# Kernel tuning notes

Hardware: AMD Instinct MI355X
Metric: run time of the kernel (lower is better)

Reference implementation:

```python
import jax, jax.numpy as jnp
import numpy as np

N = 20000   # nodes
E = 320000  # edges (before self-loops)
D = 256     # feature width (inChl = hdChl = outChl)
H = 4       # heads
C = D // H  # per-head channels = 64
NEG_SLOPE = 0.2
LN_EPS = 1e-5


def setup_inputs() -> dict:
    key = jax.random.key(0)
    ks = jax.random.split(key, 2 + 4 * 4)
    inp = {}
    inp["x"] = jax.random.normal(ks[0], (1, N, D), dtype=jnp.float32)
    inp["edge_index"] = jax.random.randint(ks[1], (2, E), 0, N, dtype=jnp.int32)
    s = 1.0 / np.sqrt(D)
    for i in range(4):
        k = 2 + 4 * i
        inp[f"Wl{i+1}"] = (jax.random.normal(ks[k], (D, H * C), dtype=jnp.float32) * s)
        inp[f"Wr{i+1}"] = (jax.random.normal(ks[k + 1], (D, H * C), dtype=jnp.float32) * s)
        inp[f"att{i+1}"] = (jax.random.normal(ks[k + 2], (H, C), dtype=jnp.float32) * s)
        inp[f"b{i+1}"] = jnp.zeros((H * C,), dtype=jnp.float32)
        inp[f"g{i+1}"] = jnp.ones((D,), dtype=jnp.float32)
        inp[f"be{i+1}"] = jnp.zeros((D,), dtype=jnp.float32)
    return inp


def _segment_softmax(scores, seg, num_segments):
    # scores: [E, H], per-destination softmax over incoming edges
    m = jax.ops.segment_max(scores, seg, num_segments=num_segments)
    e = jnp.exp(scores - m[seg])
    d = jax.ops.segment_sum(e, seg, num_segments=num_segments)
    return e / d[seg]


def _gatv2(x, src, dst, Wl, Wr, att, b):
    # GATv2Conv defaults: share_weights=False, concat=True, negative_slope=0.2
    n = x.shape[0]
    xl = (x @ Wl).reshape(n, H, C)  # source transform
    xr = (x @ Wr).reshape(n, H, C)  # target transform
    m = xl[src] + xr[dst]                                  # [E', H, C]
    e = jnp.sum(jax.nn.leaky_relu(m, NEG_SLOPE) * att, -1) # [E', H]
    alpha = _segment_softmax(e, dst, n)                    # [E', H]
    out = jax.ops.segment_sum(xl[src] * alpha[:, :, None], dst, num_segments=n)
    return out.reshape(n, H * C) + b


def _layernorm(x, g, b):
    mu = jnp.mean(x, -1, keepdims=True)
    var = jnp.mean(jnp.square(x - mu), -1, keepdims=True)
    return (x - mu) * jax.lax.rsqrt(var + LN_EPS) * g + b


def _forward(x, edge_index, layers):
    h = x[0]  # squeeze batch dim -> [N, D]
    n = h.shape[0]
    loop = jnp.arange(n, dtype=edge_index.dtype)
    src = jnp.concatenate([edge_index[0], loop])  # add_self_loops=True
    dst = jnp.concatenate([edge_index[1], loop])
    for (Wl, Wr, att, b, g, be) in layers:
        h = _gatv2(h, src, dst, Wl, Wr, att, b)
        h = jax.nn.relu(_layernorm(h, g, be))
    return h[None]  # unsqueeze -> [1, N, D]


def reference(x, edge_index,
              Wl1, Wr1, att1, b1, g1, be1,
              Wl2, Wr2, att2, b2, g2, be2,
              Wl3, Wr3, att3, b3, g3, be3,
              Wl4, Wr4, att4, b4, g4, be4):
    layers = [(Wl1, Wr1, att1, b1, g1, be1),
              (Wl2, Wr2, att2, b2, g2, be2),
              (Wl3, Wr3, att3, b3, g3, be3),
              (Wl4, Wr4, att4, b4, g4, be4)]
    return _forward(x, edge_index, layers)
```

## Files before the change

kernel.cpp:

```cpp
#include <hip/hip_runtime.h>
#include <math.h>

#define N_NODES 20000
#define E_EDGES 320000
#define EP (E_EDGES + N_NODES)
#define D 256
#define NHEAD 4
#define CH 64
#define NEG_SLOPE 0.2f
#define LN_EPS 1e-5f

typedef _Float16 half8_t __attribute__((ext_vector_type(8)));
typedef _Float16 half4_t __attribute__((ext_vector_type(4)));
typedef _Float16 half2_t __attribute__((ext_vector_type(2)));
typedef float   float4_t __attribute__((ext_vector_type(4)));

#define SCATTER_BLOCKS ((EP + 255) / 256)

__device__ __forceinline__ void async_cp16(const void* g, void* l)
{
    __builtin_amdgcn_global_load_lds(
        (const __attribute__((address_space(1))) void*)g,
        (__attribute__((address_space(3))) void*)l, 16, 0, 0);
}

template<int CTRL>
__device__ __forceinline__ float dpp_add(float v) {
    int t = __builtin_amdgcn_update_dpp(0, __float_as_int(v), CTRL, 0xF, 0xF, true);
    return v + __int_as_float(t);
}
__device__ __forceinline__ float row_sum16(float v) {
    v = dpp_add<0x121>(v);
    v = dpp_add<0x122>(v);
    v = dpp_add<0x124>(v);
    v = dpp_add<0x128>(v);
    return v;
}

__global__ __launch_bounds__(256)
void convert_hist_kernel(const float* __restrict__ x, _Float16* __restrict__ h16,
                         const int* __restrict__ ei, int* __restrict__ deg)
{
    int i = blockIdx.x * 256 + threadIdx.x;
    if (i < EP) {
        int dst = (i < E_EDGES) ? ei[E_EDGES + i] : (i - E_EDGES);
        atomicAdd(&deg[dst], 1);
    }
    if (i >= N_NODES * D / 4) return;
    float4 v = reinterpret_cast<const float4*>(x)[i];
    half4_t o;
    o.x = (_Float16)v.x; o.y = (_Float16)v.y; o.z = (_Float16)v.z; o.w = (_Float16)v.w;
    reinterpret_cast<half4_t*>(h16)[i] = o;
}

__global__ __launch_bounds__(1024)
void csr_scan_kernel(const int* __restrict__ deg, int* __restrict__ rowptr,
                     int* __restrict__ cursor, int* __restrict__ csr_src)
{
    __shared__ int wsum[16];
    int t = threadIdx.x, lane = t & 63, w = t >> 6;
    if (t < 8) csr_src[EP + t] = 0;
    int base = t * 20;
    int loc[20];
    int s = 0;
    #pragma unroll
    for (int k = 0; k < 20; ++k) {
        int idx = base + k;
        loc[k] = (idx < N_NODES) ? deg[idx] : 0;
        s += loc[k];
    }
    int x = s;
    #pragma unroll
    for (int o = 1; o < 64; o <<= 1) {
        int y = __shfl_up(x, o, 64);
        if (lane >= o) x += y;
    }
    if (lane == 63) wsum[w] = x;
    __syncthreads();
    if (t == 0) {
        int sacc = 0;
        #pragma unroll
        for (int k = 0; k < 16; ++k) { int tmp = wsum[k]; wsum[k] = sacc; sacc += tmp; }
        rowptr[N_NODES] = sacc;
    }
    __syncthreads();
    int excl = wsum[w] + x - s;
    #pragma unroll
    for (int k = 0; k < 20; ++k) {
        int idx = base + k;
        if (idx < N_NODES) { rowptr[idx] = excl; cursor[idx] = excl; }
        excl += loc[k];
    }
}

struct WPtrs { const float* p[8]; };
__global__ __launch_bounds__(256)
void scatter_convw_kernel(const int* __restrict__ ei, int* __restrict__ cursor,
                          int* __restrict__ csr_src, WPtrs wp,
                          _Float16* __restrict__ Wt_all)
{
    if (blockIdx.x < SCATTER_BLOCKS) {
        int e = blockIdx.x * 256 + threadIdx.x;
        if (e >= EP) return;
        int src, dst;
        if (e < E_EDGES) { src = ei[e]; dst = ei[E_EDGES + e]; }
        else             { src = dst = e - E_EDGES; }
        int pos = atomicAdd(&cursor[dst], 1);
        csr_src[pos] = src;
        return;
    }
    __shared__ float tile[64][65];
    int bz = blockIdx.x - SCATTER_BLOCKS;
    int bxi = bz & 3, byi = (bz >> 2) & 3, z = bz >> 4;
    const float* W = wp.p[z];
    _Float16* out = Wt_all + (size_t)z * 65536;
    int bx = bxi * 64, by = byi * 64;
    int t = threadIdx.x;
    #pragma unroll
    for (int i = 0; i < 16; ++i) {
        int idx = t + i * 256;
        int kk = idx >> 6, nn = idx & 63;
        tile[kk][nn] = W[(by + kk) * 256 + bx + nn];
    }
    __syncthreads();
    #pragma unroll
    for (int i = 0; i < 16; ++i) {
        int idx = t + i * 256;
        int nn = idx >> 6, kk = idx & 63;
        out[(bx + nn) * 256 + by + kk] = (_Float16)tile[kk][nn];
    }
}

#define BM 128
#define BN 128
#define BK 64
#define EPAD2 72
__global__ __launch_bounds__(256)
void gemm_f16_kernel(const _Float16* __restrict__ A16, const _Float16* __restrict__ Wt,
                     _Float16* __restrict__ X0, _Float16* __restrict__ X1, int nrows)
{
    const _Float16* W = Wt + blockIdx.z * 65536 + blockIdx.y * (BN * 256);
    _Float16* X = blockIdx.z ? X1 : X0;
    const int row0 = blockIdx.x * BM;
    const int col0 = blockIdx.y * BN;

    __shared__ __align__(1024) char smem[BM * BK * 2 + BN * BK * 2];
    _Float16 (*As)[BK] = reinterpret_cast<_Float16 (*)[BK]>(smem);
    _Float16 (*Bs)[BK] = reinterpret_cast<_Float16 (*)[BK]>(smem + BM * BK * 2);
    _Float16* As_flat = reinterpret_cast<_Float16*>(smem);
    _Float16* Bs_flat = reinterpret_cast<_Float16*>(smem + BM * BK * 2);
    _Float16* ep = reinterpret_cast<_Float16*>(smem);

    const int tid  = threadIdx.x;
    const int wave = tid >> 6, lane = tid & 63;
    const int wy = wave >> 1, wx = wave & 1;
    const int quad = lane >> 4, l16 = lane & 15;

    float4_t acc[4][4];
    #pragma unroll
    for (int i = 0; i < 4; ++i)
        #pragma unroll
        for (int j = 0; j < 4; ++j) acc[i][j] = (float4_t)0.0f;

    const int r_in  = lane >> 3;
    const int c_in  = (lane & 7) * 8;

    #pragma unroll
    for (int k0 = 0; k0 < 256; k0 += BK) {
        #pragma unroll
        for (int j = 0; j < 4; ++j) {
            int ia  = wave * 4 + j;
            int row = ia * 8 + r_in;
            int gra = row0 + row;
            gra = (gra < nrows) ? gra : (nrows - 1);
            async_cp16(A16 + (size_t)gra * 256 + k0 + c_in, As_flat + ia * 512);
            async_cp16(W   + (size_t)row * 256 + k0 + c_in, Bs_flat + ia * 512);
        }
        __syncthreads();

        #pragma unroll
        for (int s = 0; s < 2; ++s) {
            half8_t af[4], bf[4];
            #pragma unroll
            for (int i = 0; i < 4; ++i)
                af[i] = *reinterpret_cast<const half8_t*>(&As[wy * 64 + i * 16 + l16][s * 32 + quad * 8]);
            #pragma unroll
            for (int j = 0; j < 4; ++j)
                bf[j] = *reinterpret_cast<const half8_t*>(&Bs[wx * 64 + j * 16 + l16][s * 32 + quad * 8]);
            #pragma unroll
            for (int i = 0; i < 4; ++i)
                #pragma unroll
                for (int j = 0; j < 4; ++j)
                    acc[i][j] = __builtin_amdgcn_mfma_f32_16x16x32_f16(af[i], bf[j], acc[i][j], 0, 0, 0);
        }
        __syncthreads();
    }

    _Float16* epw = ep + wave * 16 * EPAD2;
    #pragma unroll
    for (int it = 0; it < 4; ++it) {
        #pragma unroll
        for (int j = 0; j < 4; ++j)
            #pragma unroll
            for (int r = 0; r < 4; ++r)
                epw[(quad * 4 + r) * EPAD2 + j * 16 + l16] = (_Float16)acc[it][j][r];
        #pragma unroll
        for (int p = 0; p < 2; ++p) {
            int row = p * 8 + (lane >> 3);
            int col = (lane & 7) * 8;
            int gr = row0 + wy * 64 + it * 16 + row;
            half8_t v = *reinterpret_cast<const half8_t*>(&epw[row * EPAD2 + col]);
            if (gr < nrows)
                *reinterpret_cast<half8_t*>(X + gr * 256 + col0 + wx * 64 + col) = v;
        }
    }
}

__global__ __launch_bounds__(256)
void gat_fused_kernel(const _Float16* __restrict__ xl, const _Float16* __restrict__ xr,
                      const int* __restrict__ rowptr, const int* __restrict__ csr_src,
                      const float* __restrict__ att,
                      const float* __restrict__ bias, const float* __restrict__ g,
                      const float* __restrict__ be,
                      float* __restrict__ out32, _Float16* __restrict__ out16,
                      int write32)
{
    const int tid = threadIdx.x;
    const int w = tid >> 6, lane = tid & 63;
    const int n = blockIdx.x * 4 + w;
    const int start = rowptr[n], end = rowptr[n + 1];
    const int c0 = lane * 4;

    half2_t xr01, xr23, att01, att23;
    {
        half4_t xh = *reinterpret_cast<const half4_t*>(xr + n * D + c0);
        xr01.x = xh.x; xr01.y = xh.y; xr23.x = xh.z; xr23.y = xh.w;
        float4 av = *reinterpret_cast<const float4*>(att + c0);
        att01.x = (_Float16)av.x; att01.y = (_Float16)av.y;
        att23.x = (_Float16)av.z; att23.y = (_Float16)av.w;
    }
    const half2_t k02 = {(_Float16)NEG_SLOPE, (_Float16)NEG_SLOPE};

    float den = 0.0f;
    float4 num = make_float4(0.0f, 0.0f, 0.0f, 0.0f);

    int i = start;
    for (; i + 8 <= end; i += 8) {
        int sidx[8];
        #pragma unroll
        for (int j = 0; j < 8; ++j) sidx[j] = csr_src[i + j];
        half4_t h[8];
        #pragma unroll
        for (int j = 0; j < 8; ++j)
            h[j] = *reinterpret_cast<const half4_t*>(xl + sidx[j] * D + c0);
        float p[8];
        #pragma unroll
        for (int j = 0; j < 8; ++j) {
            half2_t a01 = {h[j].x, h[j].y}, a23 = {h[j].z, h[j].w};
            half2_t t0 = a01 + xr01, t1 = a23 + xr23;
            t0 = __builtin_elementwise_max(t0, t0 * k02);
            t1 = __builtin_elementwise_max(t1, t1 * k02);
            float v = __builtin_amdgcn_fdot2(t0, att01, 0.0f, false);
            p[j]    = __builtin_amdgcn_fdot2(t1, att23, v,   false);
        }
        #pragma unroll
        for (int j = 0; j < 8; ++j) p[j] = row_sum16(p[j]);
        #pragma unroll
        for (int j = 0; j < 8; ++j) p[j] = __expf(p[j]);
        #pragma unroll
        for (int j = 0; j < 8; ++j) {
            den += p[j];
            num.x = fmaf(p[j], (float)h[j].x, num.x);
            num.y = fmaf(p[j], (float)h[j].y, num.y);
            num.z = fmaf(p[j], (float)h[j].z, num.z);
            num.w = fmaf(p[j], (float)h[j].w, num.w);
        }
    }
    for (; i < end; i += 4) {
        int sidx[4];
        #pragma unroll
        for (int j = 0; j < 4; ++j) sidx[j] = csr_src[i + j];
        half4_t h[4];
        #pragma unroll
        for (int j = 0; j < 4; ++j)
            h[j] = *reinterpret_cast<const half4_t*>(xl + sidx[j] * D + c0);
        float p[4];
        #pragma unroll
        for (int j = 0; j < 4; ++j) {
            half2_t a01 = {h[j].x, h[j].y}, a23 = {h[j].z, h[j].w};
            half2_t t0 = a01 + xr01, t1 = a23 + xr23;
            t0 = __builtin_elementwise_max(t0, t0 * k02);
            t1 = __builtin_elementwise_max(t1, t1 * k02);
            float v = __builtin_amdgcn_fdot2(t0, att01, 0.0f, false);
            p[j]    = __builtin_amdgcn_fdot2(t1, att23, v,   false);
        }
        #pragma unroll
        for (int j = 0; j < 4; ++j) p[j] = row_sum16(p[j]);
        #pragma unroll
        for (int j = 0; j < 4; ++j) {
            float pj = (i + j < end) ? __expf(p[j]) : 0.0f;
            den += pj;
            num.x = fmaf(pj, (float)h[j].x, num.x);
            num.y = fmaf(pj, (float)h[j].y, num.y);
            num.z = fmaf(pj, (float)h[j].z, num.z);
            num.w = fmaf(pj, (float)h[j].w, num.w);
        }
    }

    float inv_den = 1.0f / den;
    float4 bi = *reinterpret_cast<const float4*>(bias + c0);
    float a0 = fmaf(num.x, inv_den, bi.x);
    float a1 = fmaf(num.y, inv_den, bi.y);
    float a2 = fmaf(num.z, inv_den, bi.z);
    float a3 = fmaf(num.w, inv_den, bi.w);

    float wsum = a0 + a1 + a2 + a3;
    float wsq  = a0 * a0 + a1 * a1 + a2 * a2 + a3 * a3;
    #pragma unroll
    for (int o = 1; o < 64; o <<= 1) {
        wsum += __shfl_xor(wsum, o, 64);
        wsq  += __shfl_xor(wsq,  o, 64);
    }
    float mu = wsum * (1.0f / 256.0f);
    float var = wsq * (1.0f / 256.0f) - mu * mu;
    float rstd = rsqrtf(var + LN_EPS);

    float4 gg = *reinterpret_cast<const float4*>(g + c0);
    float4 bb = *reinterpret_cast<const float4*>(be + c0);
    float o0 = fmaxf((a0 - mu) * rstd * gg.x + bb.x, 0.0f);
    float o1 = fmaxf((a1 - mu) * rstd * gg.y + bb.y, 0.0f);
    float o2 = fmaxf((a2 - mu) * rstd * gg.z + bb.z, 0.0f);
    float o3 = fmaxf((a3 - mu) * rstd * gg.w + bb.w, 0.0f);

    if (write32) {
        float4 o4 = make_float4(o0, o1, o2, o3);
        *reinterpret_cast<float4*>(out32 + n * D + c0) = o4;
    } else {
        half4_t o4;
        o4.x = (_Float16)o0; o4.y = (_Float16)o1; o4.z = (_Float16)o2; o4.w = (_Float16)o3;
        *reinterpret_cast<half4_t*>(out16 + n * D + c0) = o4;
    }
}

extern "C" void kernel_launch(void* const* d_in, const int* in_sizes, int n_in,
                              void* d_out, int out_size, void* d_ws, size_t ws_size,
                              hipStream_t stream)
{
    const float* x  = (const float*)d_in[0];
    const int*   ei = (const int*)d_in[1];

    char* ws = (char*)d_ws;
    size_t off = 0;
    _Float16* h16   = (_Float16*)(ws + off); off += (size_t)N_NODES * D * 2;
    _Float16* xl    = (_Float16*)(ws + off); off += (size_t)N_NODES * D * 2;
    _Float16* xr    = (_Float16*)(ws + off); off += (size_t)N_NODES * D * 2;
    _Float16* WtA   = (_Float16*)(ws + off); off += (size_t)8 * 65536 * 2;
    int* rowptr     = (int*)(ws + off);      off += (size_t)(N_NODES + 32) * 4;
    int* cursor     = (int*)(ws + off);      off += (size_t)N_NODES * 4;
    int* csr_src    = (int*)(ws + off);      off += (size_t)(EP + 32) * 4;

    WPtrs wp;
    for (int l = 0; l < 4; ++l) {
        wp.p[2 * l + 0] = (const float*)d_in[2 + 6 * l + 0];
        wp.p[2 * l + 1] = (const float*)d_in[2 + 6 * l + 1];
    }

    hipMemsetAsync(cursor, 0, (size_t)N_NODES * 4, stream);
    convert_hist_kernel<<<(N_NODES * D / 4 + 255) / 256, 256, 0, stream>>>(x, h16, ei, cursor);
    csr_scan_kernel<<<1, 1024, 0, stream>>>(cursor, rowptr, cursor, csr_src);
    scatter_convw_kernel<<<SCATTER_BLOCKS + 128, 256, 0, stream>>>(ei, cursor, csr_src, wp, WtA);

    dim3 gemm_grid((N_NODES + BM - 1) / BM, 256 / BN, 2);

    for (int l = 0; l < 4; ++l) {
        const float* att  = (const float*)d_in[2 + 6 * l + 2];
        const float* bias = (const float*)d_in[2 + 6 * l + 3];
        const float* g    = (const float*)d_in[2 + 6 * l + 4];
        const float* be   = (const float*)d_in[2 + 6 * l + 5];

        gemm_f16_kernel<<<gemm_grid, 256, 0, stream>>>(h16, WtA + (size_t)l * 131072,
                                                       xl, xr, N_NODES);
        gat_fused_kernel<<<N_NODES / 4, 256, 0, stream>>>(xl, xr, rowptr, csr_src, att,
                                                          bias, g, be,
                                                          (float*)d_out, h16, (l == 3) ? 1 : 0);
    }
}
```

Measured before the change: 347.5 us.

## Remap GEMM block indices for cache locality and coalesce CSR scan via LDS

Replaces the 3D GEMM grid with a 1D grid of 640 blocks and a custom index mapping. Groups of 8 consecutive blocks share the same row tile across the xl and xr weight halves, which is intended to improve L2 reuse of the A rows, and excess blocks exit early. Rewrites the single-block CSR prefix scan to load degrees in four chunks through shared memory with coalesced global reads and writes, instead of strided per-thread runs of 20. The scan adds extra barriers and a serial carry between chunks.

Result: faster. 329.5 us (-5.2%).

```diff
diff --git a/kernel.cpp b/kernel.cpp
--- a/kernel.cpp
+++ b/kernel.cpp
@@ -57,40 +57,55 @@
 void csr_scan_kernel(const int* __restrict__ deg, int* __restrict__ rowptr,
                      int* __restrict__ cursor, int* __restrict__ csr_src)
 {
+    __shared__ int buf[5120];
     __shared__ int wsum[16];
+    __shared__ int carry_s;
     int t = threadIdx.x, lane = t & 63, w = t >> 6;
+    if (t == 0) carry_s = 0;
     if (t < 8) csr_src[EP + t] = 0;
-    int base = t * 20;
-    int loc[20];
-    int s = 0;
-    #pragma unroll
-    for (int k = 0; k < 20; ++k) {
-        int idx = base + k;
-        loc[k] = (idx < N_NODES) ? deg[idx] : 0;
-        s += loc[k];
-    }
-    int x = s;
-    #pragma unroll
-    for (int o = 1; o < 64; o <<= 1) {
-        int y = __shfl_up(x, o, 64);
-        if (lane >= o) x += y;
-    }
-    if (lane == 63) wsum[w] = x;
-    __syncthreads();
-    if (t == 0) {
-        int sacc = 0;
-        #pragma unroll
-        for (int k = 0; k < 16; ++k) { int tmp = wsum[k]; wsum[k] = sacc; sacc += tmp; }
-        rowptr[N_NODES] = sacc;
-    }
-    __syncthreads();
-    int excl = wsum[w] + x - s;
-    #pragma unroll
-    for (int k = 0; k < 20; ++k) {
-        int idx = base + k;
-        if (idx < N_NODES) { rowptr[idx] = excl; cursor[idx] = excl; }
-        excl += loc[k];
-    }
+
+    for (int c = 0; c < 4; ++c) {
+        int base = c * 5120;
+        #pragma unroll
+        for (int k = 0; k < 5; ++k) {
+            int idx = base + k * 1024 + t;
+            buf[k * 1024 + t] = (idx < N_NODES) ? deg[idx] : 0;
+        }
+        __syncthreads();
+        int loc[5]; int s = 0;
+        #pragma unroll
+        for (int k = 0; k < 5; ++k) { loc[k] = buf[t * 5 + k]; s += loc[k]; }
+        int x = s;
+        #pragma unroll
+        for (int o = 1; o < 64; o <<= 1) {
+            int y = __shfl_up(x, o, 64);
+            if (lane >= o) x += y;
+        }
+        if (lane == 63) wsum[w] = x;
+        __syncthreads();
+        if (t == 0) {
+            int sa = carry_s;
+            #pragma unroll
+            for (int k = 0; k < 16; ++k) { int tmp = wsum[k]; wsum[k] = sa; sa += tmp; }
+            carry_s = sa;
+        }
+        __syncthreads();
+        int excl = wsum[w] + x - s;
+        #pragma unroll
+        for (int k = 0; k < 5; ++k) { buf[t * 5 + k] = excl; excl += loc[k]; }
+        __syncthreads();
+        #pragma unroll
+        for (int k = 0; k < 5; ++k) {
+            int idx = base + k * 1024 + t;
+            if (idx < N_NODES) {
+                int v = buf[k * 1024 + t];
+                rowptr[idx] = v;
+                cursor[idx] = v;
+            }
+        }
+        __syncthreads();
+    }
+    if (t == 0) rowptr[N_NODES] = carry_s;
 }
 
 struct WPtrs { const float* p[8]; };
@@ -139,10 +154,17 @@
 void gemm_f16_kernel(const _Float16* __restrict__ A16, const _Float16* __restrict__ Wt,
                      _Float16* __restrict__ X0, _Float16* __restrict__ X1, int nrows)
 {
-    const _Float16* W = Wt + blockIdx.z * 65536 + blockIdx.y * (BN * 256);
-    _Float16* X = blockIdx.z ? X1 : X0;
-    const int row0 = blockIdx.x * BM;
-    const int col0 = blockIdx.y * BN;
+    const int b = blockIdx.x;
+    const int pair = ((b >> 4) << 3) + (b & 7);
+    const int z = (b >> 3) & 1;
+    if (pair >= 314) return;
+    const int yb = (pair >= 157) ? 1 : 0;
+    const int xb = pair - yb * 157;
+
+    const _Float16* W = Wt + z * 65536 + yb * (BN * 256);
+    _Float16* X = z ? X1 : X0;
+    const int row0 = xb * BM;
+    const int col0 = yb * BN;
 
     __shared__ __align__(1024) char smem[BM * BK * 2 + BN * BK * 2];
     _Float16 (*As)[BK] = reinterpret_cast<_Float16 (*)[BK]>(smem);
@@ -370,16 +392,14 @@
     csr_scan_kernel<<<1, 1024, 0, stream>>>(cursor, rowptr, cursor, csr_src);
     scatter_convw_kernel<<<SCATTER_BLOCKS + 128, 256, 0, stream>>>(ei, cursor, csr_src, wp, WtA);
 
-    dim3 gemm_grid((N_NODES + BM - 1) / BM, 256 / BN, 2);
-
     for (int l = 0; l < 4; ++l) {
         const float* att  = (const float*)d_in[2 + 6 * l + 2];
         const float* bias = (const float*)d_in[2 + 6 * l + 3];
         const float* g    = (const float*)d_in[2 + 6 * l + 4];
         const float* be   = (const float*)d_in[2 + 6 * l + 5];
 
-        gemm_f16_kernel<<<gemm_grid, 256, 0, stream>>>(h16, WtA + (size_t)l * 131072,
-                                                       xl, xr, N_NODES);
+        gemm_f16_kernel<<<640, 256, 0, stream>>>(h16, WtA + (size_t)l * 131072,
+                                                 xl, xr, N_NODES);
         gat_fused_kernel<<<N_NODES / 4, 256, 0, stream>>>(xl, xr, rowptr, csr_src, att,
                                                           bias, g, be,
                                                           (float*)d_out, h16, (l == 3) ? 1 : 0);
```
